# Performance work log

Measured on AMD Instinct MI355X. Metric: run time of the kernel, lower is better.

Reference implementation:

```python
import jax, jax.numpy as jnp
import numpy as np

EPS = 1e-07
N, Q = 1368, 21
WS = [16, 32, 64]
ST = [4, 8, 16]
OC = [64, 128, 256]


def _num_pos(n, w, s):
    return int((n - w) / s - EPS) + 1


def setup_inputs() -> dict:
    key = jax.random.key(0)
    kx, k0, k1, k2 = jax.random.split(key, 4)
    B = 64
    x = jax.random.normal(kx, (B, Q, N), dtype=jnp.float32)
    ws = []
    for kk, (w, s, d) in zip([k0, k1, k2], zip(WS, ST, OC)):
        P = _num_pos(N, w, s)
        # xavier-style small init, shape (Nk, q*w) as in FilterbankLinear.weight
        scale = np.sqrt(2.0 / (Q * w + d)).astype(np.float32)
        ws.append(scale * jax.random.normal(kk, (d * P, Q * w), dtype=jnp.float32))
    return {"x": x, "w0": ws[0], "w1": ws[1], "w2": ws[2]}


def _filterbank_linear(x, W, w, s, d):
    # x: (B, q, N); W: (d*P, q*w)
    B, q, n = x.shape
    P = _num_pos(n, w, s)
    # window starts: j*s for j in range(P-1), last window anchored at n-w
    starts = np.concatenate([np.arange(P - 1) * s, np.array([n - w])])
    idx = starts[:, None] + np.arange(w)            # (P, w) static gather indices
    win = x[:, :, idx]                              # (B, q, P, w)
    win = jnp.transpose(win, (0, 2, 1, 3)).reshape(B, P, q * w)  # (B, P, q*w), channel-major like fbank
    h = jnp.einsum('bpf,pdf->bpd', win, W.reshape(P, d, q * w))
    return h.reshape(B, P * d)


def reference(x, w0, w1, w2):
    # FilterbankEdge.forward(x, sample=False): concat of each FilterbankLinear output
    outs = [
        _filterbank_linear(x, W, w, s, d)
        for W, (w, s, d) in zip([w0, w1, w2], zip(WS, ST, OC))
    ]
    return jnp.concatenate(outs, axis=-1)  # (B, 64000)
```

## Files before the change

kernel.cpp:

```cpp
#include <hip/hip_runtime.h>

#define QDIM 21
#define NDIM 1368
#define QN (QDIM * NDIM)
#define OUTSTRIDE 64000
#define XTOT (64 * QN)

typedef __attribute__((ext_vector_type(4))) float f32x4;
typedef __attribute__((ext_vector_type(8))) short bf16x8s;
typedef __attribute__((ext_vector_type(4))) unsigned int u32x4;

typedef __attribute__((address_space(1))) const unsigned int* gas_p;
typedef __attribute__((address_space(3))) unsigned int* las_p;

static __device__ __forceinline__ void gload16(const void* g, char* l) {
    __builtin_amdgcn_global_load_lds((gas_p)g, (las_p)(void*)l, 16, 0, 0);
}

static __device__ __forceinline__ unsigned int pk2(float lo, float hi) {
    unsigned int a = __float_as_uint(lo) + 0x8000u;
    unsigned int b = __float_as_uint(hi) + 0x8000u;
    return __builtin_amdgcn_perm(b, a, 0x07060302);
}

static __device__ __forceinline__ bf16x8s pack8(f32x4 lo, f32x4 hi) {
    u32x4 p;
    p[0] = pk2(lo[0], lo[1]);
    p[1] = pk2(lo[2], lo[3]);
    p[2] = pk2(hi[0], hi[1]);
    p[3] = pk2(hi[2], hi[3]);
    return __builtin_bit_cast(bf16x8s, p);
}

static __device__ __forceinline__ int chunk_swz(int idx, int n) {
    int xcd = idx & 7;
    int i   = idx >> 3;
    int q = n >> 3, r = n & 7;
    int base = (xcd < r) ? xcd * (q + 1) : r * (q + 1) + (xcd - r) * q;
    return base + i;
}

__global__ __launch_bounds__(256)
void xcvt(const float* __restrict__ x, unsigned short* __restrict__ xb) {
    int i = (blockIdx.x * 256 + threadIdx.x) * 8;
    if (i >= XTOT) return;
    f32x4 lo = *(const f32x4*)(x + i);
    f32x4 hi = *(const f32x4*)(x + i + 4);
    *(u32x4*)(xb + i) = __builtin_bit_cast(u32x4, pack8(lo, hi));
}

template<int WLOG2, int NTX, int D, int P, int S, int K, bool ABF16>
__device__ __forceinline__ void fbk_body(const float* __restrict__ x,
                                         const unsigned short* __restrict__ xb,
                                         const float* __restrict__ W,
                                         float* __restrict__ out, int bid,
                                         char* lds) {
    constexpr int WWIN = 1 << WLOG2;
    constexpr int G = (K + 31) / 32;
    constexpr bool TAIL = (K % 32) != 0;
    constexpr int KREM = K & 31;
    constexpr int FMAXC = (K - 4) & ~3;
    constexpr int ASTB = ABF16 ? 4096 : 8192;
    constexpr int STB  = ASTB + 4096;

    const int n0 = (bid % NTX) * 32;
    const int p  = bid / NTX;
    const int start = (p == P - 1) ? (NDIM - WWIN) : p * S;

    const int tid  = threadIdx.x;
    const int wid  = tid >> 6;
    const int lane = tid & 63;
    const int wm = wid * 32;
    const int lr = lane & 15;
    const int hi = lane >> 4;
    const int kb = hi * 8;

    const int lrow = lane >> 3;
    const int g4   = ((lane & 7) ^ lrow) * 4;
    const float* wb0 = W + (size_t)(p * D + n0 + wid * 16 + lrow) * K;
    const float* wb1 = wb0 + (size_t)8 * K;

    const unsigned short* xr0 = xb + (size_t)(wid * 32 + (lane >> 2)) * QN + start;
    const float* xf0 = x + (size_t)(wid * 32 + lrow) * QN + start;

    auto STAGE = [&](int t, int sb) {
        if constexpr (ABF16) {
            int fa = t * 32 + (lane & 3) * 8;
            if constexpr (TAIL) fa = (fa > K - 8) ? (K - 8) : fa;
            int qa = fa >> WLOG2, ja = fa & (WWIN - 1);
            const unsigned short* ga = xr0 + qa * NDIM + ja;
            char* la = lds + sb + wid * 2048;
            gload16(ga, la);
            gload16(ga + (size_t)16 * QN, la + 1024);
        } else {
            int fa = t * 32 + g4;
            if constexpr (TAIL) fa = (fa > FMAXC) ? FMAXC : fa;
            int qa = fa >> WLOG2, ja = fa & (WWIN - 1);
            const float* ga = xf0 + qa * NDIM + ja;
            char* la = lds + sb + wid * 4096;
            gload16(ga,                       la);
            gload16(ga + (size_t) 8 * QN,     la + 1024);
            gload16(ga + (size_t)16 * QN,     la + 2048);
            gload16(ga + (size_t)24 * QN,     la + 3072);
        }
        int f = t * 32 + g4;
        if constexpr (TAIL) f = (f > FMAXC) ? FMAXC : f;
        char* lb = lds + sb + ASTB + wid * 2048;
        gload16(wb0 + f, lb);
        gload16(wb1 + f, lb + 1024);
    };

    const int x7 = lr & 7;
    const int c0 = ((hi * 2)     ^ x7) * 16;
    const int c1 = ((hi * 2 + 1) ^ x7) * 16;
    const int oA0b = (wm + lr) * 64 + hi * 16;
    const int oA1b = oA0b + 16 * 64;
    const int oA0f = (wm + lr) * 128;
    const int oA1f = (wm + 16 + lr) * 128;
    const int oB0 = ASTB + lr * 128;
    const int oB1 = ASTB + (16 + lr) * 128;

    f32x4 acc[2][2] = {};

    STAGE(0, 0);
    STAGE(1, STB);

    int cs = 0;
    #pragma unroll 1
    for (int t = 0; t < G; ++t) {
        if (t + 1 < G) {
            if constexpr (ABF16) asm volatile("s_waitcnt vmcnt(4)" ::: "memory");
            else                 asm volatile("s_waitcnt vmcnt(6)" ::: "memory");
        } else {
            asm volatile("s_waitcnt vmcnt(0)" ::: "memory");
        }
        __builtin_amdgcn_sched_barrier(0);
        __builtin_amdgcn_s_barrier();
        __builtin_amdgcn_sched_barrier(0);

        const char* sb = lds + cs;
        bf16x8s A0, A1;
        if constexpr (ABF16) {
            A0 = *(const bf16x8s*)(sb + oA0b);
            A1 = *(const bf16x8s*)(sb + oA1b);
            if constexpr (TAIL) {
                if (t == G - 1 && kb >= KREM) {
                    A0 = __builtin_bit_cast(bf16x8s, (u32x4){0u, 0u, 0u, 0u});
                    A1 = A0;
                }
            }
        } else {
            f32x4 a00 = *(const f32x4*)(sb + oA0f + c0);
            f32x4 a01 = *(const f32x4*)(sb + oA0f + c1);
            f32x4 a10 = *(const f32x4*)(sb + oA1f + c0);
            f32x4 a11 = *(const f32x4*)(sb + oA1f + c1);
            if constexpr (TAIL) {
                if (t == G - 1 && kb >= KREM) {
                    f32x4 z = {0.f, 0.f, 0.f, 0.f};
                    a00 = z; a01 = z; a10 = z; a11 = z;
                }
            }
            A0 = pack8(a00, a01);
            A1 = pack8(a10, a11);
        }
        f32x4 b00 = *(const f32x4*)(sb + oB0 + c0);
        f32x4 b01 = *(const f32x4*)(sb + oB0 + c1);
        f32x4 b10 = *(const f32x4*)(sb + oB1 + c0);
        f32x4 b11 = *(const f32x4*)(sb + oB1 + c1);
        bf16x8s B0 = pack8(b00, b01);
        bf16x8s B1 = pack8(b10, b11);

        acc[0][0] = __builtin_amdgcn_mfma_f32_16x16x32_bf16(A0, B0, acc[0][0], 0, 0, 0);
        acc[0][1] = __builtin_amdgcn_mfma_f32_16x16x32_bf16(A0, B1, acc[0][1], 0, 0, 0);
        acc[1][0] = __builtin_amdgcn_mfma_f32_16x16x32_bf16(A1, B0, acc[1][0], 0, 0, 0);
        acc[1][1] = __builtin_amdgcn_mfma_f32_16x16x32_bf16(A1, B1, acc[1][1], 0, 0, 0);

        __builtin_amdgcn_sched_barrier(0);
        if (t + 2 < G) {
            int pb = (cs == 0) ? 2 * STB : cs - STB;
            STAGE(t + 2, pb);
        }
        cs = (cs == 2 * STB) ? 0 : cs + STB;
    }

    const int colbase = p * D + n0;
    #pragma unroll
    for (int mi = 0; mi < 2; ++mi) {
        #pragma unroll
        for (int ni = 0; ni < 2; ++ni) {
            int col = colbase + ni * 16 + lr;
            int rbase = wm + mi * 16 + hi * 4;
            #pragma unroll
            for (int r = 0; r < 4; ++r) {
                out[(size_t)(rbase + r) * OUTSTRIDE + col] = acc[mi][ni][r];
            }
        }
    }
}

template<bool BF>
__global__ __launch_bounds__(128, 3)
void fbk_fused(const float* __restrict__ x,  const unsigned short* __restrict__ xb,
               const float* __restrict__ w0, const float* __restrict__ w1,
               const float* __restrict__ w2, float* __restrict__ out) {
    constexpr int STB = BF ? 8192 : 12288;
    __shared__ __align__(16) char lds[3 * STB];
    const int pb = blockIdx.x;
    if (pb < 656) {
        fbk_body<6, 8, 256, 82, 16, 1344, BF>(x, xb, w2, out + 43008, chunk_swz(pb, 656), lds);
    } else if (pb < 1324) {
        fbk_body<5, 4, 128, 167, 8, 672, BF>(x, xb, w1, out + 21632, chunk_swz(pb - 656, 668), lds);
    } else {
        fbk_body<4, 2, 64, 338, 4, 336, BF>(x, xb, w0, out, chunk_swz(pb - 1324, 676), lds);
    }
}

extern "C" void kernel_launch(void* const* d_in, const int* in_sizes, int n_in,
                              void* d_out, int out_size, void* d_ws, size_t ws_size,
                              hipStream_t stream) {
    const float* x  = (const float*)d_in[0];
    const float* w0 = (const float*)d_in[1];
    const float* w1 = (const float*)d_in[2];
    const float* w2 = (const float*)d_in[3];
    float* out = (float*)d_out;
    constexpr size_t XBF_BYTES = (size_t)XTOT * 2;
    if (ws_size >= XBF_BYTES) {
        unsigned short* xbuf = (unsigned short*)d_ws;
        xcvt<<<dim3((XTOT / 8 + 255) / 256), 256, 0, stream>>>(x, xbuf);
        fbk_fused<true><<<dim3(2000), 128, 0, stream>>>(x, xbuf, w0, w1, w2, out);
    } else {
        fbk_fused<false><<<dim3(2000), 128, 0, stream>>>(x, nullptr, w0, w1, w2, out);
    }
}
```

Measured before the change: 49.71 us.

## Widen block tile to 64x64 with four waves in a 2x2 layout

Each block now covers 64 rows by 64 output columns with 256 threads arranged as a 2x2 grid of waves, instead of 64x32 with two waves. The grid drops from 2000 to 1000 blocks and the staging loads are split across four waves, so each wave issues fewer global-to-LDS copies and the wait counts are lowered to match. The goal is to reuse each staged x tile across twice as many output columns and cut redundant activation traffic. The cost is more LDS per block and fewer blocks, which may lower occupancy and load balance on the last partial wave of blocks.

```diff
diff --git a/kernel.cpp b/kernel.cpp
--- a/kernel.cpp
+++ b/kernel.cpp
@@ -54,58 +54,56 @@
                                          const unsigned short* __restrict__ xb,
                                          const float* __restrict__ W,
                                          float* __restrict__ out, int bid,
-                                         char* lds) {
+                                         char* ldsraw) {
     constexpr int WWIN = 1 << WLOG2;
     constexpr int G = (K + 31) / 32;
     constexpr bool TAIL = (K % 32) != 0;
     constexpr int KREM = K & 31;
     constexpr int FMAXC = (K - 4) & ~3;
     constexpr int ASTB = ABF16 ? 4096 : 8192;
-    constexpr int STB  = ASTB + 4096;
-
-    const int n0 = (bid % NTX) * 32;
+    constexpr int STB  = ASTB + 8192;
+
+    const int n0 = (bid % NTX) * 64;
     const int p  = bid / NTX;
     const int start = (p == P - 1) ? (NDIM - WWIN) : p * S;
 
     const int tid  = threadIdx.x;
     const int wid  = tid >> 6;
     const int lane = tid & 63;
-    const int wm = wid * 32;
+    const int wm = (wid >> 1) * 32;
+    const int wn = (wid & 1) * 32;
     const int lr = lane & 15;
     const int hi = lane >> 4;
     const int kb = hi * 8;
 
     const int lrow = lane >> 3;
     const int g4   = ((lane & 7) ^ lrow) * 4;
-    const float* wb0 = W + (size_t)(p * D + n0 + wid * 16 + lrow) * K;
+    const float* Wp  = W + (size_t)(p * D + n0) * K;
+    const float* wb0 = Wp + (size_t)(16 * wid + lrow) * K;
     const float* wb1 = wb0 + (size_t)8 * K;
-
-    const unsigned short* xr0 = xb + (size_t)(wid * 32 + (lane >> 2)) * QN + start;
-    const float* xf0 = x + (size_t)(wid * 32 + lrow) * QN + start;
-
-    auto STAGE = [&](int t, int sb) {
+    const int wB = 2048 * wid;
+
+    const unsigned short* xr0 = xb + (size_t)(16 * wid + (lane >> 2)) * QN + start;
+    const float* xf0 = x + (size_t)(16 * wid + lrow) * QN + start;
+
+    auto STAGE = [&](int t, int sbase) {
         if constexpr (ABF16) {
             int fa = t * 32 + (lane & 3) * 8;
             if constexpr (TAIL) fa = (fa > K - 8) ? (K - 8) : fa;
             int qa = fa >> WLOG2, ja = fa & (WWIN - 1);
-            const unsigned short* ga = xr0 + qa * NDIM + ja;
-            char* la = lds + sb + wid * 2048;
-            gload16(ga, la);
-            gload16(ga + (size_t)16 * QN, la + 1024);
+            gload16(xr0 + qa * NDIM + ja, ldsraw + sbase + 1024 * wid);
         } else {
             int fa = t * 32 + g4;
             if constexpr (TAIL) fa = (fa > FMAXC) ? FMAXC : fa;
             int qa = fa >> WLOG2, ja = fa & (WWIN - 1);
             const float* ga = xf0 + qa * NDIM + ja;
-            char* la = lds + sb + wid * 4096;
-            gload16(ga,                       la);
-            gload16(ga + (size_t) 8 * QN,     la + 1024);
-            gload16(ga + (size_t)16 * QN,     la + 2048);
-            gload16(ga + (size_t)24 * QN,     la + 3072);
+            char* la = ldsraw + sbase + 2048 * wid;
+            gload16(ga, la);
+            gload16(ga + (size_t)8 * QN, la + 1024);
         }
         int f = t * 32 + g4;
         if constexpr (TAIL) f = (f > FMAXC) ? FMAXC : f;
-        char* lb = lds + sb + ASTB + wid * 2048;
+        char* lb = ldsraw + sbase + ASTB + wB;
         gload16(wb0 + f, lb);
         gload16(wb1 + f, lb + 1024);
     };
@@ -114,11 +112,11 @@
     const int c0 = ((hi * 2)     ^ x7) * 16;
     const int c1 = ((hi * 2 + 1) ^ x7) * 16;
     const int oA0b = (wm + lr) * 64 + hi * 16;
-    const int oA1b = oA0b + 16 * 64;
+    const int oA1b = oA0b + 1024;
     const int oA0f = (wm + lr) * 128;
     const int oA1f = (wm + 16 + lr) * 128;
-    const int oB0 = ASTB + lr * 128;
-    const int oB1 = ASTB + (16 + lr) * 128;
+    const int oB0 = ASTB + (wn + lr) * 128;
+    const int oB1 = ASTB + (wn + 16 + lr) * 128;
 
     f32x4 acc[2][2] = {};
 
@@ -129,8 +127,8 @@
     #pragma unroll 1
     for (int t = 0; t < G; ++t) {
         if (t + 1 < G) {
-            if constexpr (ABF16) asm volatile("s_waitcnt vmcnt(4)" ::: "memory");
-            else                 asm volatile("s_waitcnt vmcnt(6)" ::: "memory");
+            if constexpr (ABF16) asm volatile("s_waitcnt vmcnt(3)" ::: "memory");
+            else                 asm volatile("s_waitcnt vmcnt(4)" ::: "memory");
         } else {
             asm volatile("s_waitcnt vmcnt(0)" ::: "memory");
         }
@@ -138,7 +136,7 @@
         __builtin_amdgcn_s_barrier();
         __builtin_amdgcn_sched_barrier(0);
 
-        const char* sb = lds + cs;
+        const char* sb = ldsraw + cs;
         bf16x8s A0, A1;
         if constexpr (ABF16) {
             A0 = *(const bf16x8s*)(sb + oA0b);
@@ -188,7 +186,7 @@
     for (int mi = 0; mi < 2; ++mi) {
         #pragma unroll
         for (int ni = 0; ni < 2; ++ni) {
-            int col = colbase + ni * 16 + lr;
+            int col = colbase + wn + ni * 16 + lr;
             int rbase = wm + mi * 16 + hi * 4;
             #pragma unroll
             for (int r = 0; r < 4; ++r) {
@@ -199,19 +197,19 @@
 }
 
 template<bool BF>
-__global__ __launch_bounds__(128, 3)
+__global__ __launch_bounds__(256, 4)
 void fbk_fused(const float* __restrict__ x,  const unsigned short* __restrict__ xb,
                const float* __restrict__ w0, const float* __restrict__ w1,
                const float* __restrict__ w2, float* __restrict__ out) {
-    constexpr int STB = BF ? 8192 : 12288;
-    __shared__ __align__(16) char lds[3 * STB];
+    constexpr int STB = BF ? 12288 : 16384;
+    __shared__ __align__(16) char ldsraw[3 * STB];
     const int pb = blockIdx.x;
-    if (pb < 656) {
-        fbk_body<6, 8, 256, 82, 16, 1344, BF>(x, xb, w2, out + 43008, chunk_swz(pb, 656), lds);
-    } else if (pb < 1324) {
-        fbk_body<5, 4, 128, 167, 8, 672, BF>(x, xb, w1, out + 21632, chunk_swz(pb - 656, 668), lds);
+    if (pb < 328) {
+        fbk_body<6, 4, 256, 82, 16, 1344, BF>(x, xb, w2, out + 43008, chunk_swz(pb, 328), ldsraw);
+    } else if (pb < 662) {
+        fbk_body<5, 2, 128, 167, 8, 672, BF>(x, xb, w1, out + 21632, chunk_swz(pb - 328, 334), ldsraw);
     } else {
-        fbk_body<4, 2, 64, 338, 4, 336, BF>(x, xb, w0, out, chunk_swz(pb - 1324, 676), lds);
+        fbk_body<4, 1, 64, 338, 4, 336, BF>(x, xb, w0, out, chunk_swz(pb - 662, 338), ldsraw);
     }
 }
 
@@ -227,8 +225,8 @@
     if (ws_size >= XBF_BYTES) {
         unsigned short* xbuf = (unsigned short*)d_ws;
         xcvt<<<dim3((XTOT / 8 + 255) / 256), 256, 0, stream>>>(x, xbuf);
-        fbk_fused<true><<<dim3(2000), 128, 0, stream>>>(x, xbuf, w0, w1, w2, out);
+        fbk_fused<true><<<dim3(1000), 256, 0, stream>>>(x, xbuf, w0, w1, w2, out);
     } else {
-        fbk_fused<false><<<dim3(2000), 128, 0, stream>>>(x, nullptr, w0, w1, w2, out);
-    }
-}
+        fbk_fused<false><<<dim3(1000), 256, 0, stream>>>(x, nullptr, w0, w1, w2, out);
+    }
+}
```

Result: faster. 45.34 us (-8.8%).
